# Optimization experiments

Hardware: AMD Instinct MI355X
Metric: run time of the kernel (lower is better)

## Reference

```python
import jax, jax.numpy as jnp
import numpy as np

N = 100000      # nodes
E = 1600000     # edges
F_IN = 165      # elliptic node features
H = 128         # hidden channels
OUT = 2         # classes


def setup_inputs() -> dict:
    key = jax.random.key(0)
    ks = jax.random.split(key, 8)
    x = jax.random.normal(ks[0], (N, F_IN), dtype=jnp.float32)
    edge_index = jax.random.randint(ks[1], (2, E), 0, N, dtype=jnp.int32)
    def glorot(k, fan_in, fan_out):
        s = 1.0 / np.sqrt(fan_in)
        return jax.random.uniform(k, (fan_in, fan_out), jnp.float32, -s, s)
    W1 = glorot(ks[2], F_IN, H); b1 = jnp.zeros((H,), jnp.float32)
    W2 = glorot(ks[3], H, H);    b2 = jnp.zeros((H,), jnp.float32)
    W3 = glorot(ks[4], H, OUT);  b3 = jnp.zeros((OUT,), jnp.float32)
    return {"x": x, "edge_index": edge_index,
            "W1": W1, "b1": b1, "W2": W2, "b2": b2, "W3": W3, "b3": b3}


def _gcn_layer(x, W, b, src, dst):
    # PyG GCNConv: h = x @ W; symmetric norm with added self-loops; agg + bias.
    h = x @ W                                    # [N, H]
    n = x.shape[0]
    deg = jax.ops.segment_sum(jnp.ones((src.shape[0],), h.dtype), dst,
                              num_segments=n) + 1.0   # +1 for self-loop
    dinv = jax.lax.rsqrt(deg)                    # deg >= 1 always
    norm = dinv[src] * dinv[dst]                 # [E]
    msg = h[src] * norm[:, None]                 # [E, H]  (gather)
    agg = jax.ops.segment_sum(msg, dst, num_segments=n)   # scatter-add
    agg = agg + h * (dinv * dinv)[:, None]       # self-loop contribution
    return agg + b


def reference(x, edge_index, W1, b1, W2, b2, W3, b3):
    src, dst = edge_index[0], edge_index[1]
    h = jax.nn.relu(_gcn_layer(x, W1, b1, src, dst))
    # dropout: identity in eval mode
    h = jax.nn.relu(_gcn_layer(h, W2, b2, src, dst))
    return h @ W3 + b3                           # [N, OUT]
```

## Files before the change

kernel.cpp:

```cpp
#include <hip/hip_runtime.h>
#include <hip/hip_fp16.h>


constexpr int NN   = 100000;
constexpr int NE   = 1600000;
constexpr int FIN  = 165;
constexpr int HID  = 128;
constexpr int CAP  = 64;
constexpr int NPX  = NN / 8;
constexpr int NCHUNK = 250;
constexpr int EPC  = (NE + NCHUNK - 1) / NCHUNK;
constexpr int K2_1 = (FIN + 1) / 2;
constexpr int NB_G = (NN + 63) / 64;

typedef _Float16 h2v __attribute__((ext_vector_type(2)));

__device__ __forceinline__ float fdot2u(unsigned a, unsigned b, float c) {
#if __has_builtin(__builtin_amdgcn_fdot2)
    return __builtin_amdgcn_fdot2(__builtin_bit_cast(h2v, a),
                                  __builtin_bit_cast(h2v, b), c, false);
#else
    __half2 ah = __builtin_bit_cast(__half2, a);
    __half2 bh = __builtin_bit_cast(__half2, b);
    float2 af = __half22float2(ah), bf = __half22float2(bh);
    return fmaf(af.x, bf.x, fmaf(af.y, bf.y, c));
#endif
}

__global__ __launch_bounds__(256) void k_zero_cur(int* __restrict__ cur) {
    int i = blockIdx.x * 256 + threadIdx.x;
    if (i < NN) cur[i] = 0;
}

__global__ __launch_bounds__(256) void k_wpack(const float* __restrict__ W1,
                                               const float* __restrict__ W2,
                                               unsigned* __restrict__ W1p,
                                               unsigned* __restrict__ W2p) {
    int idx = blockIdx.x * 256 + threadIdx.x;
    if (idx < 64 * 128) {
        int k2 = idx >> 7, c = idx & 127;
        __half2 h = __floats2half2_rn(W2[(2 * k2) * HID + c],
                                      W2[(2 * k2 + 1) * HID + c]);
        W2p[idx] = __builtin_bit_cast(unsigned, h);
    } else {
        int j = idx - 64 * 128;
        if (j >= K2_1 * HID) return;
        int k2 = j / HID, c = j % HID;
        float lo = W1[(2 * k2) * HID + c];
        float hi = (2 * k2 + 1 < FIN) ? W1[(2 * k2 + 1) * HID + c] : 0.0f;
        __half2 h = __floats2half2_rn(lo, hi);
        W1p[j] = __builtin_bit_cast(unsigned, h);
    }
}

__global__ __launch_bounds__(256) void k_fill_pad(const int* __restrict__ src,
                                                  const int* __restrict__ dst,
                                                  int* __restrict__ cur,
                                                  int* __restrict__ col) {
    const int b  = blockIdx.x;
    const int lo = (b & 7) * NPX;
    const int hi = lo + NPX;
    const int q  = b >> 3;
    const int e0 = q * EPC;
    const int e1 = (e0 + EPC < NE) ? e0 + EPC : NE;

    int e = e0 + threadIdx.x;
    for (; e + 3 * 256 < e1; e += 4 * 256) {
        int d0 = __builtin_nontemporal_load(&dst[e]);
        int d1 = __builtin_nontemporal_load(&dst[e + 256]);
        int d2 = __builtin_nontemporal_load(&dst[e + 512]);
        int d3 = __builtin_nontemporal_load(&dst[e + 768]);
        int s0 = __builtin_nontemporal_load(&src[e]);
        int s1 = __builtin_nontemporal_load(&src[e + 256]);
        int s2 = __builtin_nontemporal_load(&src[e + 512]);
        int s3 = __builtin_nontemporal_load(&src[e + 768]);
        if (d0 >= lo && d0 < hi) col[d0 * CAP + atomicAdd(&cur[d0], 1)] = s0;
        if (d1 >= lo && d1 < hi) col[d1 * CAP + atomicAdd(&cur[d1], 1)] = s1;
        if (d2 >= lo && d2 < hi) col[d2 * CAP + atomicAdd(&cur[d2], 1)] = s2;
        if (d3 >= lo && d3 < hi) col[d3 * CAP + atomicAdd(&cur[d3], 1)] = s3;
    }
    for (; e < e1; e += 256) {
        int d = __builtin_nontemporal_load(&dst[e]);
        if (d >= lo && d < hi) {
            int s = __builtin_nontemporal_load(&src[e]);
            col[d * CAP + atomicAdd(&cur[d], 1)] = s;
        }
    }
}

__global__ __launch_bounds__(256) void k_gemm1(const float* __restrict__ X,
                                               const unsigned* __restrict__ W1p,
                                               const int* __restrict__ cnt,
                                               __half* __restrict__ Yh) {
    constexpr int K = FIN;
    constexpr int KPH = 168;
    constexpr int KPU = 84;
    __shared__ __half Xs[64 * KPH];
    const int tid = threadIdx.x;
    const long base = (long)blockIdx.x * 64;
    const int rows = (NN - base < 64) ? (int)(NN - base) : 64;

    const float* Xg = X + base * K;
    for (int i = tid; i < rows * K; i += 256) {
        int r = i / K, c = i % K;
        Xs[r * KPH + c] = __float2half(Xg[i]);
    }
    for (int i = tid; i < 64 * 3; i += 256) {
        int r = i / 3, c = K + i % 3;
        Xs[r * KPH + c] = __float2half(0.f);
    }
    if (rows < 64) {
        for (int i = tid; i < (64 - rows) * KPH; i += 256)
            Xs[rows * KPH + i] = __float2half(0.f);
    }
    __syncthreads();

    const int cg = tid & 31;
    const int rg = tid >> 5;
    const unsigned* Wp = W1p + 4 * cg;
    const unsigned* XrowU = (const unsigned*)&Xs[rg * 8 * KPH];

    float acc[8][4];
#pragma unroll
    for (int r = 0; r < 8; ++r)
#pragma unroll
        for (int c = 0; c < 4; ++c) acc[r][c] = 0.0f;

    int k2 = 0;
    for (; k2 + 2 <= K2_1; k2 += 2) {
        uint4 w0 = *(const uint4*)(Wp + (k2 + 0) * HID);
        uint4 w1 = *(const uint4*)(Wp + (k2 + 1) * HID);
#pragma unroll
        for (int r = 0; r < 8; ++r) {
            uint2 xp = *(const uint2*)&XrowU[r * KPU + k2];
            acc[r][0] = fdot2u(xp.x, w0.x, acc[r][0]);
            acc[r][1] = fdot2u(xp.x, w0.y, acc[r][1]);
            acc[r][2] = fdot2u(xp.x, w0.z, acc[r][2]);
            acc[r][3] = fdot2u(xp.x, w0.w, acc[r][3]);
            acc[r][0] = fdot2u(xp.y, w1.x, acc[r][0]);
            acc[r][1] = fdot2u(xp.y, w1.y, acc[r][1]);
            acc[r][2] = fdot2u(xp.y, w1.z, acc[r][2]);
            acc[r][3] = fdot2u(xp.y, w1.w, acc[r][3]);
        }
    }
    {
        uint4 wt = *(const uint4*)(Wp + k2 * HID);
#pragma unroll
        for (int r = 0; r < 8; ++r) {
            unsigned xp = XrowU[r * KPU + k2];
            acc[r][0] = fdot2u(xp, wt.x, acc[r][0]);
            acc[r][1] = fdot2u(xp, wt.y, acc[r][1]);
            acc[r][2] = fdot2u(xp, wt.z, acc[r][2]);
            acc[r][3] = fdot2u(xp, wt.w, acc[r][3]);
        }
    }

#pragma unroll
    for (int r = 0; r < 8; ++r) {
        long row = base + rg * 8 + r;
        if (row < NN) {
            float d = rsqrtf((float)cnt[row] + 1.0f);
            __half2 p0 = __floats2half2_rn(acc[r][0] * d, acc[r][1] * d);
            __half2 p1 = __floats2half2_rn(acc[r][2] * d, acc[r][3] * d);
            uint2 uv;
            uv.x = *reinterpret_cast<unsigned int*>(&p0);
            uv.y = *reinterpret_cast<unsigned int*>(&p1);
            *reinterpret_cast<uint2*>(&Yh[row * HID + 4 * cg]) = uv;
        }
    }
}

__device__ __forceinline__ void gather_row_h(const __half2* __restrict__ H2,
                                             const int* __restrict__ col,
                                             int i, int cnt, int j,
                                             float& a0, float& a1) {
    const int base = i * CAP;
    float2 self = __half22float2(H2[(size_t)i * 64 + j]);
    a0 = self.x;
    a1 = self.y;
    int k = 0;
    for (; k + 8 <= cnt; k += 8) {
        int s[8];
#pragma unroll
        for (int u = 0; u < 8; ++u)
            s[u] = __builtin_nontemporal_load(&col[base + k + u]);
        __half2 h[8];
#pragma unroll
        for (int u = 0; u < 8; ++u) h[u] = H2[(size_t)s[u] * 64 + j];
#pragma unroll
        for (int u = 0; u < 8; ++u) {
            float2 f = __half22float2(h[u]);
            a0 += f.x;
            a1 += f.y;
        }
    }
    for (; k < cnt; ++k) {
        int cs = __builtin_nontemporal_load(&col[base + k]);
        float2 f = __half22float2(H2[(size_t)cs * 64 + j]);
        a0 += f.x;
        a1 += f.y;
    }
}

template<int MODE>
__global__ __launch_bounds__(64) void k_aggP(const __half* __restrict__ Hh,
                                             const int* __restrict__ cntA,
                                             const int* __restrict__ col,
                                             const float* __restrict__ bias,
                                             __half* __restrict__ Oh) {
    const int j = threadIdx.x;
    const int base = blockIdx.x * 4;
    const __half2* H2 = (const __half2*)Hh;
    float2 bb = make_float2(0.f, 0.f);
    if (MODE == 0) bb = ((const float2*)bias)[j];

#pragma unroll
    for (int n = 0; n < 4; ++n) {
        const int i = base + n;
        const int cnt = cntA[i];
        const float di = rsqrtf((float)cnt + 1.0f);
        float a0, a1;
        gather_row_h(H2, col, i, cnt, j, a0, a1);
        float r0, r1;
        if (MODE == 0) {
            r0 = di * fmaxf(di * a0 + bb.x, 0.0f);
            r1 = di * fmaxf(di * a1 + bb.y, 0.0f);
        } else {
            r0 = di * a0;
            r1 = di * a1;
        }
        ((__half2*)Oh)[(size_t)i * 64 + j] = __floats2half2_rn(r0, r1);
    }
}

__global__ __launch_bounds__(256) void k_tail(const unsigned* __restrict__ Ug,
                                              const unsigned* __restrict__ W2p,
                                              const float* __restrict__ b2,
                                              const float* __restrict__ W3,
                                              const float* __restrict__ b3,
                                              float* __restrict__ out) {
    __shared__ unsigned Xs[64 * 66];
    __shared__ unsigned Ws[64 * 128];
    const int tid = threadIdx.x;
    const long base = (long)blockIdx.x * 64;

#pragma unroll
    for (int i = 0; i < 4; ++i) {
        int li = tid + i * 256;
        int row = li >> 4;
        int q4  = li & 15;
        uint4 v = make_uint4(0, 0, 0, 0);
        if (base + row < NN)
            v = *(const uint4*)&Ug[(base + row) * 64 + q4 * 4];
        Xs[row * 66 + q4 * 4 + 0] = v.x;
        Xs[row * 66 + q4 * 4 + 1] = v.y;
        Xs[row * 66 + q4 * 4 + 2] = v.z;
        Xs[row * 66 + q4 * 4 + 3] = v.w;
    }
#pragma unroll
    for (int i = 0; i < 8; ++i) {
        int li = tid + i * 256;
        *(uint4*)&Ws[li * 4] = *(const uint4*)&W2p[li * 4];
    }
    __syncthreads();

    const int cg = tid & 31;
    const int rg = tid >> 5;

    float acc[8][4];
#pragma unroll
    for (int r = 0; r < 8; ++r)
#pragma unroll
        for (int c = 0; c < 4; ++c) acc[r][c] = 0.0f;

    for (int k2 = 0; k2 < 64; k2 += 2) {
        uint4 w0 = *(const uint4*)&Ws[k2 * 128 + 4 * cg];
        uint4 w1 = *(const uint4*)&Ws[(k2 + 1) * 128 + 4 * cg];
#pragma unroll
        for (int r = 0; r < 8; ++r) {
            uint2 xp = *(const uint2*)&Xs[(rg * 8 + r) * 66 + k2];
            acc[r][0] = fdot2u(xp.x, w0.x, acc[r][0]);
            acc[r][1] = fdot2u(xp.x, w0.y, acc[r][1]);
            acc[r][2] = fdot2u(xp.x, w0.z, acc[r][2]);
            acc[r][3] = fdot2u(xp.x, w0.w, acc[r][3]);
            acc[r][0] = fdot2u(xp.y, w1.x, acc[r][0]);
            acc[r][1] = fdot2u(xp.y, w1.y, acc[r][1]);
            acc[r][2] = fdot2u(xp.y, w1.z, acc[r][2]);
            acc[r][3] = fdot2u(xp.y, w1.w, acc[r][3]);
        }
    }

    const float4 bb = *(const float4*)&b2[4 * cg];
    float2 w3v[4];
#pragma unroll
    for (int c = 0; c < 4; ++c)
        w3v[c] = *(const float2*)&W3[(4 * cg + c) * 2];
    const float b30 = b3[0], b31 = b3[1];

#pragma unroll
    for (int r = 0; r < 8; ++r) {
        float h0 = fmaxf(acc[r][0] + bb.x, 0.f);
        float h1 = fmaxf(acc[r][1] + bb.y, 0.f);
        float h2 = fmaxf(acc[r][2] + bb.z, 0.f);
        float h3 = fmaxf(acc[r][3] + bb.w, 0.f);
        float p0 = h0 * w3v[0].x + h1 * w3v[1].x + h2 * w3v[2].x + h3 * w3v[3].x;
        float p1 = h0 * w3v[0].y + h1 * w3v[1].y + h2 * w3v[2].y + h3 * w3v[3].y;
#pragma unroll
        for (int m = 1; m < 32; m <<= 1) {
            p0 += __shfl_xor(p0, m);
            p1 += __shfl_xor(p1, m);
        }
        long row = base + rg * 8 + r;
        if (cg == 0 && row < NN)
            ((float2*)out)[row] = make_float2(p0 + b30, p1 + b31);
    }
}

extern "C" void kernel_launch(void* const* d_in, const int* in_sizes, int n_in,
                              void* d_out, int out_size, void* d_ws, size_t ws_size,
                              hipStream_t stream) {
    const float* x   = (const float*)d_in[0];
    const int*   ei  = (const int*)d_in[1];
    const float* W1  = (const float*)d_in[2];
    const float* b1  = (const float*)d_in[3];
    const float* W2  = (const float*)d_in[4];
    const float* b2  = (const float*)d_in[5];
    const float* W3  = (const float*)d_in[6];
    const float* b3  = (const float*)d_in[7];
    float* out = (float*)d_out;

    const int* srcA = ei;
    const int* dstA = ei + NE;

    char* p = (char*)d_ws;
    auto alloc = [&](size_t bytes) {
        char* r = p;
        p += (bytes + 255) & ~(size_t)255;
        return r;
    };
    int*      cur    = (int*)  alloc(NN * 4);
    int*      col    = (int*)  alloc((size_t)NN * CAP * 4);
    unsigned* w2pk   = (unsigned*)alloc(64 * 128 * 4);
    unsigned* w1pk   = (unsigned*)alloc(K2_1 * HID * 4);
    __half*   hhat   = (__half*)alloc((size_t)NN * HID * 2);
    __half*   h2hat  = (__half*)alloc((size_t)NN * HID * 2);
    __half*   ubuf   = (__half*)alloc((size_t)NN * HID * 2);

    const int nb_n = (NN + 255) / 256;
    const int nb_wp = (64 * 128 + K2_1 * HID + 255) / 256;

    k_zero_cur<<<nb_n, 256, 0, stream>>>(cur);
    k_wpack<<<nb_wp, 256, 0, stream>>>(W1, W2, w1pk, w2pk);
    k_fill_pad<<<8 * NCHUNK, 256, 0, stream>>>(srcA, dstA, cur, col);

    k_gemm1<<<NB_G, 256, 0, stream>>>(x, w1pk, cur, hhat);

    k_aggP<0><<<NN / 4, 64, 0, stream>>>(hhat, cur, col, b1, h2hat);

    k_aggP<1><<<NN / 4, 64, 0, stream>>>(h2hat, cur, col, nullptr, ubuf);

    k_tail<<<NB_G, 256, 0, stream>>>((const unsigned*)ubuf, w2pk, b2, W3, b3, out);
}
```

Before: 309.5 us.

## Replace 8-pass edge filtering with two-phase bucket-then-scatter CSR build

The old fill kernel read the full edge list eight times, once per destination range, so that atomics to the padded adjacency stayed localized. The new path reads edges once. It bins them into 8 destination buckets in a temp buffer, packing the source index and local destination into one word. A second kernel then scatters each bucket into the padded column array. Zeroing of the per-node counters is folded into the bucket kernel, and the bucket counters are zeroed in the weight-pack kernel. This removes repeated edge reads and one launch, but adds a temp buffer round trip and assumes each bucket holds at most 210000 edges and that sources fit in 17 bits.

```diff
diff --git a/kernel.cpp b/kernel.cpp
--- a/kernel.cpp
+++ b/kernel.cpp
@@ -8,10 +8,13 @@
 constexpr int HID  = 128;
 constexpr int CAP  = 64;
 constexpr int NPX  = NN / 8;
-constexpr int NCHUNK = 250;
-constexpr int EPC  = (NE + NCHUNK - 1) / NCHUNK;
 constexpr int K2_1 = (FIN + 1) / 2;
 constexpr int NB_G = (NN + 63) / 64;
+constexpr int BKCAP = 210000;
+constexpr int EPB1 = 2048;
+constexpr int NB1  = (NE + EPB1 - 1) / EPB1;
+constexpr int EPB2 = 2048;
+constexpr int NB2C = (BKCAP + EPB2 - 1) / EPB2;
 
 typedef _Float16 h2v __attribute__((ext_vector_type(2)));
 
@@ -27,16 +30,13 @@
 #endif
 }
 
-__global__ __launch_bounds__(256) void k_zero_cur(int* __restrict__ cur) {
-    int i = blockIdx.x * 256 + threadIdx.x;
-    if (i < NN) cur[i] = 0;
-}
-
 __global__ __launch_bounds__(256) void k_wpack(const float* __restrict__ W1,
                                                const float* __restrict__ W2,
                                                unsigned* __restrict__ W1p,
-                                               unsigned* __restrict__ W2p) {
+                                               unsigned* __restrict__ W2p,
+                                               int* __restrict__ bcur) {
     int idx = blockIdx.x * 256 + threadIdx.x;
+    if (idx < 8) bcur[idx] = 0;
     if (idx < 64 * 128) {
         int k2 = idx >> 7, c = idx & 127;
         __half2 h = __floats2half2_rn(W2[(2 * k2) * HID + c],
@@ -53,38 +53,84 @@
     }
 }
 
-__global__ __launch_bounds__(256) void k_fill_pad(const int* __restrict__ src,
-                                                  const int* __restrict__ dst,
+__global__ __launch_bounds__(256) void k_bucket8(const int* __restrict__ src,
+                                                 const int* __restrict__ dst,
+                                                 int* __restrict__ bcur,
+                                                 unsigned* __restrict__ tmp,
+                                                 int* __restrict__ cur) {
+    __shared__ int lcnt[8];
+    __shared__ int lbase[8];
+    const int b = blockIdx.x;
+    const int t = threadIdx.x;
+    {
+        int z = b * 128 + (t & 127);
+        if (t < 128 && z < NN) cur[z] = 0;
+    }
+    if (t < 8) lcnt[t] = 0;
+    __syncthreads();
+    const int e0 = b * EPB1;
+    const int e1 = (e0 + EPB1 < NE) ? e0 + EPB1 : NE;
+
+    int myb[8], myp[8], myr[8];
+    bool ok[8];
+#pragma unroll
+    for (int u = 0; u < 8; ++u) {
+        int e = e0 + t + u * 256;
+        ok[u] = (e < e1);
+        myb[u] = 0; myp[u] = 0; myr[u] = 0;
+        if (ok[u]) {
+            int d = __builtin_nontemporal_load(&dst[e]);
+            int s = __builtin_nontemporal_load(&src[e]);
+            int bk = (int)((unsigned)d / (unsigned)NPX);
+            int dl = d - bk * NPX;
+            myb[u] = bk;
+            myp[u] = s | (dl << 17);
+            myr[u] = atomicAdd(&lcnt[bk], 1);
+        }
+    }
+    __syncthreads();
+    if (t < 8) lbase[t] = atomicAdd(&bcur[t], lcnt[t]);
+    __syncthreads();
+#pragma unroll
+    for (int u = 0; u < 8; ++u) {
+        if (ok[u]) {
+            int bk = myb[u];
+            tmp[(size_t)bk * BKCAP + lbase[bk] + myr[u]] = (unsigned)myp[u];
+        }
+    }
+}
+
+__global__ __launch_bounds__(256) void k_scatter8(const unsigned* __restrict__ tmp,
+                                                  const int* __restrict__ bcur,
                                                   int* __restrict__ cur,
                                                   int* __restrict__ col) {
-    const int b  = blockIdx.x;
-    const int lo = (b & 7) * NPX;
-    const int hi = lo + NPX;
-    const int q  = b >> 3;
-    const int e0 = q * EPC;
-    const int e1 = (e0 + EPC < NE) ? e0 + EPC : NE;
-
-    int e = e0 + threadIdx.x;
-    for (; e + 3 * 256 < e1; e += 4 * 256) {
-        int d0 = __builtin_nontemporal_load(&dst[e]);
-        int d1 = __builtin_nontemporal_load(&dst[e + 256]);
-        int d2 = __builtin_nontemporal_load(&dst[e + 512]);
-        int d3 = __builtin_nontemporal_load(&dst[e + 768]);
-        int s0 = __builtin_nontemporal_load(&src[e]);
-        int s1 = __builtin_nontemporal_load(&src[e + 256]);
-        int s2 = __builtin_nontemporal_load(&src[e + 512]);
-        int s3 = __builtin_nontemporal_load(&src[e + 768]);
-        if (d0 >= lo && d0 < hi) col[d0 * CAP + atomicAdd(&cur[d0], 1)] = s0;
-        if (d1 >= lo && d1 < hi) col[d1 * CAP + atomicAdd(&cur[d1], 1)] = s1;
-        if (d2 >= lo && d2 < hi) col[d2 * CAP + atomicAdd(&cur[d2], 1)] = s2;
-        if (d3 >= lo && d3 < hi) col[d3 * CAP + atomicAdd(&cur[d3], 1)] = s3;
-    }
-    for (; e < e1; e += 256) {
-        int d = __builtin_nontemporal_load(&dst[e]);
-        if (d >= lo && d < hi) {
-            int s = __builtin_nontemporal_load(&src[e]);
-            col[d * CAP + atomicAdd(&cur[d], 1)] = s;
-        }
+    const int bk = blockIdx.x & 7;
+    const int ch = blockIdx.x >> 3;
+    const int cnt = bcur[bk];
+    const int i0 = ch * EPB2;
+    if (i0 >= cnt) return;
+    const int i1 = (i0 + EPB2 < cnt) ? i0 + EPB2 : cnt;
+    const unsigned* tb = tmp + (size_t)bk * BKCAP;
+    const int dbase = bk * NPX;
+    int i = i0 + threadIdx.x;
+    for (; i + 3 * 256 < i1; i += 4 * 256) {
+        unsigned p0 = tb[i];
+        unsigned p1 = tb[i + 256];
+        unsigned p2 = tb[i + 512];
+        unsigned p3 = tb[i + 768];
+        int d0 = dbase + (int)(p0 >> 17);
+        int d1 = dbase + (int)(p1 >> 17);
+        int d2 = dbase + (int)(p2 >> 17);
+        int d3 = dbase + (int)(p3 >> 17);
+        col[d0 * CAP + atomicAdd(&cur[d0], 1)] = (int)(p0 & 0x1FFFFu);
+        col[d1 * CAP + atomicAdd(&cur[d1], 1)] = (int)(p1 & 0x1FFFFu);
+        col[d2 * CAP + atomicAdd(&cur[d2], 1)] = (int)(p2 & 0x1FFFFu);
+        col[d3 * CAP + atomicAdd(&cur[d3], 1)] = (int)(p3 & 0x1FFFFu);
+    }
+    for (; i < i1; i += 256) {
+        unsigned pk = tb[i];
+        int d = dbase + (int)(pk >> 17);
+        col[d * CAP + atomicAdd(&cur[d], 1)] = (int)(pk & 0x1FFFFu);
     }
 }
 
@@ -339,6 +385,8 @@
         return r;
     };
     int*      cur    = (int*)  alloc(NN * 4);
+    int*      bcur   = (int*)  alloc(8 * 4);
+    unsigned* tmp    = (unsigned*)alloc((size_t)8 * BKCAP * 4);
     int*      col    = (int*)  alloc((size_t)NN * CAP * 4);
     unsigned* w2pk   = (unsigned*)alloc(64 * 128 * 4);
     unsigned* w1pk   = (unsigned*)alloc(K2_1 * HID * 4);
@@ -346,12 +394,13 @@
     __half*   h2hat  = (__half*)alloc((size_t)NN * HID * 2);
     __half*   ubuf   = (__half*)alloc((size_t)NN * HID * 2);
 
-    const int nb_n = (NN + 255) / 256;
     const int nb_wp = (64 * 128 + K2_1 * HID + 255) / 256;
 
-    k_zero_cur<<<nb_n, 256, 0, stream>>>(cur);
-    k_wpack<<<nb_wp, 256, 0, stream>>>(W1, W2, w1pk, w2pk);
-    k_fill_pad<<<8 * NCHUNK, 256, 0, stream>>>(srcA, dstA, cur, col);
+    k_wpack<<<nb_wp, 256, 0, stream>>>(W1, W2, w1pk, w2pk, bcur);
+
+    k_bucket8<<<NB1, 256, 0, stream>>>(srcA, dstA, bcur, tmp, cur);
+
+    k_scatter8<<<8 * NB2C, 256, 0, stream>>>(tmp, bcur, cur, col);
 
     k_gemm1<<<NB_G, 256, 0, stream>>>(x, w1pk, cur, hhat);
 
```

After: 314.9 us. About the same (+1.7%).

## Use MFMA 16x16x32 f16 instructions for the first-layer GEMM

Applied to the files above, without the earlier changes.

Replaces the packed-dot2 scalar GEMM for X@W1 with a matrix-core version built on mfma_f32_16x16x32_f16. W1 is repacked into 8-half K blocks, padded to 192 in K, to match the MFMA B-operand layout, and X is staged in shared memory with a wider padded stride. Each wave computes a 16x128 output tile. The cost is strided scalar half stores in the epilogue and some wasted padded K work.

```diff
diff --git a/kernel.cpp b/kernel.cpp
--- a/kernel.cpp
+++ b/kernel.cpp
@@ -10,10 +10,12 @@
 constexpr int NPX  = NN / 8;
 constexpr int NCHUNK = 250;
 constexpr int EPC  = (NE + NCHUNK - 1) / NCHUNK;
-constexpr int K2_1 = (FIN + 1) / 2;
 constexpr int NB_G = (NN + 63) / 64;
-
-typedef _Float16 h2v __attribute__((ext_vector_type(2)));
+constexpr int KBLK = 24;
+
+typedef _Float16 h2v  __attribute__((ext_vector_type(2)));
+typedef _Float16 f16x8 __attribute__((ext_vector_type(8)));
+typedef float    f32x4 __attribute__((ext_vector_type(4)));
 
 __device__ __forceinline__ float fdot2u(unsigned a, unsigned b, float c) {
 #if __has_builtin(__builtin_amdgcn_fdot2)
@@ -34,7 +36,7 @@
 
 __global__ __launch_bounds__(256) void k_wpack(const float* __restrict__ W1,
                                                const float* __restrict__ W2,
-                                               unsigned* __restrict__ W1p,
+                                               uint4* __restrict__ Wb,
                                                unsigned* __restrict__ W2p) {
     int idx = blockIdx.x * 256 + threadIdx.x;
     if (idx < 64 * 128) {
@@ -44,12 +46,18 @@
         W2p[idx] = __builtin_bit_cast(unsigned, h);
     } else {
         int j = idx - 64 * 128;
-        if (j >= K2_1 * HID) return;
-        int k2 = j / HID, c = j % HID;
-        float lo = W1[(2 * k2) * HID + c];
-        float hi = (2 * k2 + 1 < FIN) ? W1[(2 * k2 + 1) * HID + c] : 0.0f;
-        __half2 h = __floats2half2_rn(lo, hi);
-        W1p[j] = __builtin_bit_cast(unsigned, h);
+        if (j >= KBLK * HID) return;
+        int kb = j >> 7, c = j & 127;
+        unsigned u[4];
+#pragma unroll
+        for (int q = 0; q < 4; ++q) {
+            int k0 = kb * 8 + 2 * q;
+            float lo = (k0     < FIN) ? W1[(size_t)k0 * HID + c] : 0.0f;
+            float hi = (k0 + 1 < FIN) ? W1[(size_t)(k0 + 1) * HID + c] : 0.0f;
+            __half2 h = __floats2half2_rn(lo, hi);
+            u[q] = __builtin_bit_cast(unsigned, h);
+        }
+        Wb[j] = make_uint4(u[0], u[1], u[2], u[3]);
     }
 }
 
@@ -88,84 +96,65 @@
     }
 }
 
-__global__ __launch_bounds__(256) void k_gemm1(const float* __restrict__ X,
-                                               const unsigned* __restrict__ W1p,
-                                               const int* __restrict__ cnt,
-                                               __half* __restrict__ Yh) {
-    constexpr int K = FIN;
-    constexpr int KPH = 168;
-    constexpr int KPU = 84;
+__global__ __launch_bounds__(256) void k_gemm1m(const float* __restrict__ X,
+                                                const uint4* __restrict__ Wb,
+                                                const int* __restrict__ cnt,
+                                                __half* __restrict__ Yh) {
+    constexpr int KPH = 200;
     __shared__ __half Xs[64 * KPH];
     const int tid = threadIdx.x;
     const long base = (long)blockIdx.x * 64;
     const int rows = (NN - base < 64) ? (int)(NN - base) : 64;
 
-    const float* Xg = X + base * K;
-    for (int i = tid; i < rows * K; i += 256) {
-        int r = i / K, c = i % K;
-        Xs[r * KPH + c] = __float2half(Xg[i]);
-    }
-    for (int i = tid; i < 64 * 3; i += 256) {
-        int r = i / 3, c = K + i % 3;
-        Xs[r * KPH + c] = __float2half(0.f);
+    for (int i = tid; i < rows * FIN; i += 256) {
+        int r = i / FIN, c = i % FIN;
+        Xs[r * KPH + c] = __float2half(X[base * FIN + i]);
+    }
+    for (int i = tid; i < 64 * 27; i += 256) {
+        int r = i / 27, c = FIN + i % 27;
+        Xs[r * KPH + c] = __float2half(0.0f);
     }
     if (rows < 64) {
         for (int i = tid; i < (64 - rows) * KPH; i += 256)
-            Xs[rows * KPH + i] = __float2half(0.f);
+            Xs[rows * KPH + i] = __float2half(0.0f);
     }
     __syncthreads();
 
-    const int cg = tid & 31;
-    const int rg = tid >> 5;
-    const unsigned* Wp = W1p + 4 * cg;
-    const unsigned* XrowU = (const unsigned*)&Xs[rg * 8 * KPH];
-
-    float acc[8][4];
-#pragma unroll
-    for (int r = 0; r < 8; ++r)
-#pragma unroll
-        for (int c = 0; c < 4; ++c) acc[r][c] = 0.0f;
-
-    int k2 = 0;
-    for (; k2 + 2 <= K2_1; k2 += 2) {
-        uint4 w0 = *(const uint4*)(Wp + (k2 + 0) * HID);
-        uint4 w1 = *(const uint4*)(Wp + (k2 + 1) * HID);
-#pragma unroll
-        for (int r = 0; r < 8; ++r) {
-            uint2 xp = *(const uint2*)&XrowU[r * KPU + k2];
-            acc[r][0] = fdot2u(xp.x, w0.x, acc[r][0]);
-            acc[r][1] = fdot2u(xp.x, w0.y, acc[r][1]);
-            acc[r][2] = fdot2u(xp.x, w0.z, acc[r][2]);
-            acc[r][3] = fdot2u(xp.x, w0.w, acc[r][3]);
-            acc[r][0] = fdot2u(xp.y, w1.x, acc[r][0]);
-            acc[r][1] = fdot2u(xp.y, w1.y, acc[r][1]);
-            acc[r][2] = fdot2u(xp.y, w1.z, acc[r][2]);
-            acc[r][3] = fdot2u(xp.y, w1.w, acc[r][3]);
-        }
-    }
-    {
-        uint4 wt = *(const uint4*)(Wp + k2 * HID);
-#pragma unroll
-        for (int r = 0; r < 8; ++r) {
-            unsigned xp = XrowU[r * KPU + k2];
-            acc[r][0] = fdot2u(xp, wt.x, acc[r][0]);
-            acc[r][1] = fdot2u(xp, wt.y, acc[r][1]);
-            acc[r][2] = fdot2u(xp, wt.z, acc[r][2]);
-            acc[r][3] = fdot2u(xp, wt.w, acc[r][3]);
-        }
-    }
-
-#pragma unroll
-    for (int r = 0; r < 8; ++r) {
-        long row = base + rg * 8 + r;
-        if (row < NN) {
-            float d = rsqrtf((float)cnt[row] + 1.0f);
-            __half2 p0 = __floats2half2_rn(acc[r][0] * d, acc[r][1] * d);
-            __half2 p1 = __floats2half2_rn(acc[r][2] * d, acc[r][3] * d);
-            uint2 uv;
-            uv.x = *reinterpret_cast<unsigned int*>(&p0);
-            uv.y = *reinterpret_cast<unsigned int*>(&p1);
-            *reinterpret_cast<uint2*>(&Yh[row * HID + 4 * cg]) = uv;
+    const int w   = tid >> 6;
+    const int l   = tid & 63;
+    const int l16 = l & 15;
+    const int lq  = l >> 4;
+
+    f32x4 acc[8];
+#pragma unroll
+    for (int n = 0; n < 8; ++n) acc[n] = (f32x4){0.f, 0.f, 0.f, 0.f};
+
+    const __half* Arow = &Xs[(16 * w + l16) * KPH + lq * 8];
+#pragma unroll
+    for (int s = 0; s < 6; ++s) {
+        f16x8 a = *(const f16x8*)(Arow + s * 32);
+        const uint4* bp = &Wb[(4 * s + lq) * HID + l16];
+#pragma unroll
+        for (int n = 0; n < 8; ++n) {
+            f16x8 b = __builtin_bit_cast(f16x8, bp[16 * n]);
+            acc[n] = __builtin_amdgcn_mfma_f32_16x16x32_f16(a, b, acc[n], 0, 0, 0);
+        }
+    }
+
+    long rowR[4];
+    float dR[4];
+#pragma unroll
+    for (int reg = 0; reg < 4; ++reg) {
+        rowR[reg] = base + 16 * w + lq * 4 + reg;
+        dR[reg] = (rowR[reg] < NN) ? rsqrtf((float)cnt[rowR[reg]] + 1.0f) : 0.f;
+    }
+#pragma unroll
+    for (int n = 0; n < 8; ++n) {
+        int colc = 16 * n + l16;
+#pragma unroll
+        for (int reg = 0; reg < 4; ++reg) {
+            if (rowR[reg] < NN)
+                Yh[rowR[reg] * HID + colc] = __float2half(acc[n][reg] * dR[reg]);
         }
     }
 }
@@ -341,19 +330,19 @@
     int*      cur    = (int*)  alloc(NN * 4);
     int*      col    = (int*)  alloc((size_t)NN * CAP * 4);
     unsigned* w2pk   = (unsigned*)alloc(64 * 128 * 4);
-    unsigned* w1pk   = (unsigned*)alloc(K2_1 * HID * 4);
+    uint4*    wb4    = (uint4*)alloc((size_t)KBLK * HID * 16);
     __half*   hhat   = (__half*)alloc((size_t)NN * HID * 2);
     __half*   h2hat  = (__half*)alloc((size_t)NN * HID * 2);
     __half*   ubuf   = (__half*)alloc((size_t)NN * HID * 2);
 
-    const int nb_n = (NN + 255) / 256;
-    const int nb_wp = (64 * 128 + K2_1 * HID + 255) / 256;
+    const int nb_n  = (NN + 255) / 256;
+    const int nb_wp = (64 * 128 + KBLK * HID + 255) / 256;
 
     k_zero_cur<<<nb_n, 256, 0, stream>>>(cur);
-    k_wpack<<<nb_wp, 256, 0, stream>>>(W1, W2, w1pk, w2pk);
+    k_wpack<<<nb_wp, 256, 0, stream>>>(W1, W2, wb4, w2pk);
     k_fill_pad<<<8 * NCHUNK, 256, 0, stream>>>(srcA, dstA, cur, col);
 
-    k_gemm1<<<NB_G, 256, 0, stream>>>(x, w1pk, cur, hhat);
+    k_gemm1m<<<NB_G, 256, 0, stream>>>(x, wb4, cur, hhat);
 
     k_aggP<0><<<NN / 4, 64, 0, stream>>>(hhat, cur, col, b1, h2hat);
 
```

Measured after the change: 283.9 us. -8.3%, faster.
